# Performance work log

Measured on AMD Instinct MI355X. Metric: run time of the kernel, lower is better.

Reference implementation:

```python
import jax, jax.numpy as jnp
import numpy as np


def setup_inputs() -> dict:
    key = jax.random.key(0)
    k1, k2 = jax.random.split(key)
    B, N, M = 8, 4096, 4096
    xyz1 = jax.random.normal(k1, (B, N, 3), dtype=jnp.float32)
    xyz2 = jax.random.normal(k2, (B, M, 3), dtype=jnp.float32)
    return {"xyz1": xyz1, "xyz2": xyz2}


def _chamfer_sq_dists(xyz1, xyz2):
    # Squared euclidean all-pairs distances via ||a||^2 + ||b||^2 - 2 a.b
    # xyz1: [B,N,3], xyz2: [B,M,3]
    n1 = jnp.sum(xyz1 * xyz1, axis=-1)              # [B,N]
    n2 = jnp.sum(xyz2 * xyz2, axis=-1)              # [B,M]
    dots = jnp.einsum('bnd,bmd->bnm', xyz1, xyz2)   # [B,N,M]
    d2 = n1[:, :, None] + n2[:, None, :] - 2.0 * dots
    dist1 = jnp.min(d2, axis=2)                     # [B,N] min over xyz2
    dist2 = jnp.min(d2, axis=1)                     # [B,M] min over xyz1
    return dist1, dist2


def reference(xyz1, xyz2):
    dist1, dist2 = _chamfer_sq_dists(xyz1, xyz2)
    return jnp.mean(dist1) + jnp.mean(dist2)
```

## Files before the change

kernel.cpp:

```cpp
#include <hip/hip_runtime.h>

#define BLOCK 256
#define IPT 4
#define PTS_PER_BLOCK (BLOCK * IPT)
#define MCHUNKS 16
#define TILE_MAX 512

__global__ __launch_bounds__(BLOCK) void pack_and_init(
    const float* __restrict__ xyz1, const float* __restrict__ xyz2,
    float4* __restrict__ pk, unsigned int* __restrict__ mins,
    int n1, int ntot) {
    int i = blockIdx.x * BLOCK + threadIdx.x;
    if (i < ntot) {
        const float* s = (i < n1) ? (xyz1 + 3 * (size_t)i) : (xyz2 + 3 * (size_t)(i - n1));
        float x = s[0], y = s[1], z = s[2];
        pk[i] = make_float4(x, y, z, fmaf(z, z, fmaf(y, y, x * x)));
        mins[i] = 0x7F7F7F7Fu;
    }
}

__global__ __launch_bounds__(BLOCK) void chamfer_min_pass(
    const float4* __restrict__ pk, unsigned int* __restrict__ mins,
    int n1, int N, int M) {
    int dir = blockIdx.z;
    const float4* own = dir ? pk + n1 : pk;
    const float4* oth = dir ? pk : pk + n1;
    unsigned int* mo = dir ? mins + n1 : mins;
    int np = dir ? M : N;
    int mp = dir ? N : M;

    int bpb = np / PTS_PER_BLOCK;
    int b = blockIdx.x / bpb;
    size_t gbase = (size_t)b * np + (blockIdx.x % bpb) * PTS_PER_BLOCK + threadIdx.x;

    float4 p0 = own[gbase + 0 * BLOCK];
    float4 p1 = own[gbase + 1 * BLOCK];
    float4 p2 = own[gbase + 2 * BLOCK];
    float4 p3 = own[gbase + 3 * BLOCK];

    int mlen = mp / MCHUNKS;
    const float4* o = oth + (size_t)b * mp + (size_t)blockIdx.y * mlen;

    __shared__ float4 tile[TILE_MAX];
    for (int t = threadIdx.x; t < mlen; t += BLOCK) tile[t] = o[t];
    __syncthreads();

    float a0 = 3.0e38f, a1 = 3.0e38f, a2 = 3.0e38f, a3 = 3.0e38f;
#pragma unroll 4
    for (int j = 0; j < mlen; ++j) {
        float4 q = tile[j];
        float d0 = fmaf(p0.z, q.z, fmaf(p0.y, q.y, p0.x * q.x));
        float d1 = fmaf(p1.z, q.z, fmaf(p1.y, q.y, p1.x * q.x));
        float d2 = fmaf(p2.z, q.z, fmaf(p2.y, q.y, p2.x * q.x));
        float d3 = fmaf(p3.z, q.z, fmaf(p3.y, q.y, p3.x * q.x));
        a0 = fminf(a0, fmaf(-2.0f, d0, q.w));
        a1 = fminf(a1, fmaf(-2.0f, d1, q.w));
        a2 = fminf(a2, fmaf(-2.0f, d2, q.w));
        a3 = fminf(a3, fmaf(-2.0f, d3, q.w));
    }
    atomicMin(mo + gbase + 0 * BLOCK, __float_as_uint(fmaxf(a0 + p0.w, 0.0f)));
    atomicMin(mo + gbase + 1 * BLOCK, __float_as_uint(fmaxf(a1 + p1.w, 0.0f)));
    atomicMin(mo + gbase + 2 * BLOCK, __float_as_uint(fmaxf(a2 + p2.w, 0.0f)));
    atomicMin(mo + gbase + 3 * BLOCK, __float_as_uint(fmaxf(a3 + p3.w, 0.0f)));
}

__global__ __launch_bounds__(BLOCK) void reduce_means(
    const unsigned int* __restrict__ mins, int n1, int ntot,
    float inv1, float inv2, float* __restrict__ out) {
    float s = 0.0f;
    for (int i = blockIdx.x * BLOCK + threadIdx.x; i < ntot; i += gridDim.x * BLOCK) {
        float v = __uint_as_float(mins[i]);
        s += v * (i < n1 ? inv1 : inv2);
    }
    for (int off = 32; off; off >>= 1) s += __shfl_down(s, off, 64);
    __shared__ float red[BLOCK / 64];
    int lane = threadIdx.x & 63, wid = threadIdx.x >> 6;
    if (!lane) red[wid] = s;
    __syncthreads();
    if (!threadIdx.x) atomicAdd(out, red[0] + red[1] + red[2] + red[3]);
}

__global__ __launch_bounds__(BLOCK) void chamfer_direct(
    const float* __restrict__ x1, const float* __restrict__ x2,
    int Npts, int Mpts, float inv1, float inv2, float* __restrict__ out) {
    int dir = blockIdx.z;
    const float* own = dir ? x2 : x1;
    const float* oth = dir ? x1 : x2;
    int np = dir ? Mpts : Npts;
    int mp = dir ? Npts : Mpts;
    float scale = dir ? inv2 : inv1;

    int bpb = np / BLOCK;
    int b = blockIdx.x / bpb;
    int i = (blockIdx.x % bpb) * BLOCK + threadIdx.x;

    const float* pp = own + ((size_t)b * np + i) * 3;
    float px = pp[0], py = pp[1], pz = pp[2];
    const float* o = oth + (size_t)b * mp * 3;

    float best = 3.0e38f;
#pragma unroll 4
    for (int j = 0; j < mp; ++j) {
        float dx = px - o[3 * j + 0];
        float dy = py - o[3 * j + 1];
        float dz = pz - o[3 * j + 2];
        float d2 = fmaf(dz, dz, fmaf(dy, dy, dx * dx));
        best = fminf(best, d2);
    }
    float s = best * scale;
    for (int off = 32; off; off >>= 1) s += __shfl_down(s, off, 64);
    __shared__ float red[BLOCK / 64];
    int lane = threadIdx.x & 63, wid = threadIdx.x >> 6;
    if (!lane) red[wid] = s;
    __syncthreads();
    if (!threadIdx.x) atomicAdd(out, red[0] + red[1] + red[2] + red[3]);
}

extern "C" void kernel_launch(void* const* d_in, const int* in_sizes, int n_in,
                              void* d_out, int out_size, void* d_ws, size_t ws_size,
                              hipStream_t stream) {
    const float* xyz1 = (const float*)d_in[0];
    const float* xyz2 = (const float*)d_in[1];
    float* out = (float*)d_out;

    const int N = 4096, M = 4096;
    const int B = in_sizes[0] / (3 * N);
    const int n1 = B * N;
    const int n2 = B * M;
    const int ntot = n1 + n2;

    hipMemsetAsync(d_out, 0, sizeof(float), stream);

    size_t minBytes = (size_t)ntot * sizeof(unsigned int);
    size_t pkBytes = (size_t)ntot * sizeof(float4);
    bool okShape = (N % PTS_PER_BLOCK == 0) && (M % PTS_PER_BLOCK == 0) &&
                   (M / MCHUNKS <= TILE_MAX) && (N / MCHUNKS <= TILE_MAX);

    if (ws_size >= minBytes + pkBytes && okShape) {
        unsigned int* mins = (unsigned int*)d_ws;
        float4* pk = (float4*)((char*)d_ws + minBytes);

        pack_and_init<<<(ntot + BLOCK - 1) / BLOCK, BLOCK, 0, stream>>>(
            xyz1, xyz2, pk, mins, n1, ntot);

        dim3 grid(B * (N / PTS_PER_BLOCK), MCHUNKS, 2);
        chamfer_min_pass<<<grid, BLOCK, 0, stream>>>(pk, mins, n1, N, M);

        reduce_means<<<64, BLOCK, 0, stream>>>(mins, n1, ntot,
                                               1.0f / (float)n1, 1.0f / (float)n2, out);
    } else {
        dim3 grid(B * (N / BLOCK), 1, 2);
        chamfer_direct<<<grid, BLOCK, 0, stream>>>(xyz1, xyz2, N, M,
                                                   1.0f / (float)n1, 1.0f / (float)n2, out);
    }
}
```

Before: 39.60 us.

## Pack inner loop with f32x2 ops over SoA shared tile, fold memset into pack kernel

Stores the shared-memory tile in structure-of-arrays form and reads four candidates per float4 load, then runs the distance and min arithmetic on 2-wide float vectors so the compiler can emit packed FP32 FMA and min instructions. It also adds a launch-bounds occupancy hint and zeroes the output inside the pack kernel instead of with a separate memset. The aim is fewer VALU instructions per pair and fewer LDS loads, plus one less launch. The tile size is now fixed at compile time, so the fast path only accepts shapes where M/16 equals 256.

```diff
diff --git a/kernel.cpp b/kernel.cpp
--- a/kernel.cpp
+++ b/kernel.cpp
@@ -1,16 +1,19 @@
 #include <hip/hip_runtime.h>
+
+typedef float f32x2 __attribute__((ext_vector_type(2)));
 
 #define BLOCK 256
 #define IPT 4
 #define PTS_PER_BLOCK (BLOCK * IPT)
 #define MCHUNKS 16
-#define TILE_MAX 512
+#define TILE 256
 
 __global__ __launch_bounds__(BLOCK) void pack_and_init(
     const float* __restrict__ xyz1, const float* __restrict__ xyz2,
     float4* __restrict__ pk, unsigned int* __restrict__ mins,
-    int n1, int ntot) {
+    int n1, int ntot, float* __restrict__ out) {
     int i = blockIdx.x * BLOCK + threadIdx.x;
+    if (i == 0) *out = 0.0f;
     if (i < ntot) {
         const float* s = (i < n1) ? (xyz1 + 3 * (size_t)i) : (xyz2 + 3 * (size_t)(i - n1));
         float x = s[0], y = s[1], z = s[2];
@@ -19,7 +22,7 @@
     }
 }
 
-__global__ __launch_bounds__(BLOCK) void chamfer_min_pass(
+__global__ __launch_bounds__(BLOCK, 4) void chamfer_min_pass(
     const float4* __restrict__ pk, unsigned int* __restrict__ mins,
     int n1, int N, int M) {
     int dir = blockIdx.z;
@@ -38,30 +41,62 @@
     float4 p2 = own[gbase + 2 * BLOCK];
     float4 p3 = own[gbase + 3 * BLOCK];
 
-    int mlen = mp / MCHUNKS;
-    const float4* o = oth + (size_t)b * mp + (size_t)blockIdx.y * mlen;
+    const float4* o = oth + (size_t)b * mp + (size_t)blockIdx.y * TILE;
 
-    __shared__ float4 tile[TILE_MAX];
-    for (int t = threadIdx.x; t < mlen; t += BLOCK) tile[t] = o[t];
+    __shared__ float smem[4][TILE];
+    for (int t = threadIdx.x; t < TILE; t += BLOCK) {
+        float4 q = o[t];
+        smem[0][t] = q.x; smem[1][t] = q.y; smem[2][t] = q.z; smem[3][t] = q.w;
+    }
     __syncthreads();
 
-    float a0 = 3.0e38f, a1 = 3.0e38f, a2 = 3.0e38f, a3 = 3.0e38f;
-#pragma unroll 4
-    for (int j = 0; j < mlen; ++j) {
-        float4 q = tile[j];
-        float d0 = fmaf(p0.z, q.z, fmaf(p0.y, q.y, p0.x * q.x));
-        float d1 = fmaf(p1.z, q.z, fmaf(p1.y, q.y, p1.x * q.x));
-        float d2 = fmaf(p2.z, q.z, fmaf(p2.y, q.y, p2.x * q.x));
-        float d3 = fmaf(p3.z, q.z, fmaf(p3.y, q.y, p3.x * q.x));
-        a0 = fminf(a0, fmaf(-2.0f, d0, q.w));
-        a1 = fminf(a1, fmaf(-2.0f, d1, q.w));
-        a2 = fminf(a2, fmaf(-2.0f, d2, q.w));
-        a3 = fminf(a3, fmaf(-2.0f, d3, q.w));
+    f32x2 px0 = {p0.x, p0.x}, py0 = {p0.y, p0.y}, pz0 = {p0.z, p0.z};
+    f32x2 px1 = {p1.x, p1.x}, py1 = {p1.y, p1.y}, pz1 = {p1.z, p1.z};
+    f32x2 px2 = {p2.x, p2.x}, py2 = {p2.y, p2.y}, pz2 = {p2.z, p2.z};
+    f32x2 px3 = {p3.x, p3.x}, py3 = {p3.y, p3.y}, pz3 = {p3.z, p3.z};
+    const f32x2 m2 = {-2.0f, -2.0f};
+
+    f32x2 a0 = {3.0e38f, 3.0e38f}, a1 = a0, a2 = a0, a3 = a0;
+
+    const float4* tx4 = (const float4*)smem[0];
+    const float4* ty4 = (const float4*)smem[1];
+    const float4* tz4 = (const float4*)smem[2];
+    const float4* tw4 = (const float4*)smem[3];
+
+#pragma unroll 2
+    for (int j = 0; j < TILE / 4; ++j) {
+        float4 qx = tx4[j], qy = ty4[j], qz = tz4[j], qw = tw4[j];
+        f32x2 qxl = {qx.x, qx.y}, qxh = {qx.z, qx.w};
+        f32x2 qyl = {qy.x, qy.y}, qyh = {qy.z, qy.w};
+        f32x2 qzl = {qz.x, qz.y}, qzh = {qz.z, qz.w};
+        f32x2 qwl = {qw.x, qw.y}, qwh = {qw.z, qw.w};
+
+        f32x2 d;
+        d = qxl * px0; d = __builtin_elementwise_fma(qyl, py0, d); d = __builtin_elementwise_fma(qzl, pz0, d);
+        a0 = __builtin_elementwise_min(a0, __builtin_elementwise_fma(d, m2, qwl));
+        d = qxh * px0; d = __builtin_elementwise_fma(qyh, py0, d); d = __builtin_elementwise_fma(qzh, pz0, d);
+        a0 = __builtin_elementwise_min(a0, __builtin_elementwise_fma(d, m2, qwh));
+
+        d = qxl * px1; d = __builtin_elementwise_fma(qyl, py1, d); d = __builtin_elementwise_fma(qzl, pz1, d);
+        a1 = __builtin_elementwise_min(a1, __builtin_elementwise_fma(d, m2, qwl));
+        d = qxh * px1; d = __builtin_elementwise_fma(qyh, py1, d); d = __builtin_elementwise_fma(qzh, pz1, d);
+        a1 = __builtin_elementwise_min(a1, __builtin_elementwise_fma(d, m2, qwh));
+
+        d = qxl * px2; d = __builtin_elementwise_fma(qyl, py2, d); d = __builtin_elementwise_fma(qzl, pz2, d);
+        a2 = __builtin_elementwise_min(a2, __builtin_elementwise_fma(d, m2, qwl));
+        d = qxh * px2; d = __builtin_elementwise_fma(qyh, py2, d); d = __builtin_elementwise_fma(qzh, pz2, d);
+        a2 = __builtin_elementwise_min(a2, __builtin_elementwise_fma(d, m2, qwh));
+
+        d = qxl * px3; d = __builtin_elementwise_fma(qyl, py3, d); d = __builtin_elementwise_fma(qzl, pz3, d);
+        a3 = __builtin_elementwise_min(a3, __builtin_elementwise_fma(d, m2, qwl));
+        d = qxh * px3; d = __builtin_elementwise_fma(qyh, py3, d); d = __builtin_elementwise_fma(qzh, pz3, d);
+        a3 = __builtin_elementwise_min(a3, __builtin_elementwise_fma(d, m2, qwh));
     }
-    atomicMin(mo + gbase + 0 * BLOCK, __float_as_uint(fmaxf(a0 + p0.w, 0.0f)));
-    atomicMin(mo + gbase + 1 * BLOCK, __float_as_uint(fmaxf(a1 + p1.w, 0.0f)));
-    atomicMin(mo + gbase + 2 * BLOCK, __float_as_uint(fmaxf(a2 + p2.w, 0.0f)));
-    atomicMin(mo + gbase + 3 * BLOCK, __float_as_uint(fmaxf(a3 + p3.w, 0.0f)));
+
+    atomicMin(mo + gbase + 0 * BLOCK, __float_as_uint(fmaxf(fminf(a0.x, a0.y) + p0.w, 0.0f)));
+    atomicMin(mo + gbase + 1 * BLOCK, __float_as_uint(fmaxf(fminf(a1.x, a1.y) + p1.w, 0.0f)));
+    atomicMin(mo + gbase + 2 * BLOCK, __float_as_uint(fmaxf(fminf(a2.x, a2.y) + p2.w, 0.0f)));
+    atomicMin(mo + gbase + 3 * BLOCK, __float_as_uint(fmaxf(fminf(a3.x, a3.y) + p3.w, 0.0f)));
 }
 
 __global__ __launch_bounds__(BLOCK) void reduce_means(
@@ -129,19 +164,17 @@
     const int n2 = B * M;
     const int ntot = n1 + n2;
 
-    hipMemsetAsync(d_out, 0, sizeof(float), stream);
-
     size_t minBytes = (size_t)ntot * sizeof(unsigned int);
     size_t pkBytes = (size_t)ntot * sizeof(float4);
     bool okShape = (N % PTS_PER_BLOCK == 0) && (M % PTS_PER_BLOCK == 0) &&
-                   (M / MCHUNKS <= TILE_MAX) && (N / MCHUNKS <= TILE_MAX);
+                   (M / MCHUNKS == TILE) && (N / MCHUNKS == TILE);
 
     if (ws_size >= minBytes + pkBytes && okShape) {
         unsigned int* mins = (unsigned int*)d_ws;
         float4* pk = (float4*)((char*)d_ws + minBytes);
 
         pack_and_init<<<(ntot + BLOCK - 1) / BLOCK, BLOCK, 0, stream>>>(
-            xyz1, xyz2, pk, mins, n1, ntot);
+            xyz1, xyz2, pk, mins, n1, ntot, out);
 
         dim3 grid(B * (N / PTS_PER_BLOCK), MCHUNKS, 2);
         chamfer_min_pass<<<grid, BLOCK, 0, stream>>>(pk, mins, n1, N, M);
@@ -149,6 +182,7 @@
         reduce_means<<<64, BLOCK, 0, stream>>>(mins, n1, ntot,
                                                1.0f / (float)n1, 1.0f / (float)n2, out);
     } else {
+        hipMemsetAsync(d_out, 0, sizeof(float), stream);
         dim3 grid(B * (N / BLOCK), 1, 2);
         chamfer_direct<<<grid, BLOCK, 0, stream>>>(xyz1, xyz2, N, M,
                                                    1.0f / (float)n1, 1.0f / (float)n2, out);
```

After: 37.65 us. 1.05x faster.

## Compute chamfer distances with bf16 split-precision MFMA and fused reduction

Applied to the files above, without the earlier changes.

Replaces the scalar FMA all-pairs loop with 32x32x16 bf16 MFMA instructions. Each coordinate is split into high and low bf16 parts so the dot product plus the other point's norm is recovered at near-fp32 accuracy. Row minima are reduced in registers and across lanes, then summed straight into the output, which removes the atomicMin buffer, the separate reduce kernel and the memset. In exchange it adds packing overhead and risks small accuracy loss, and it uses a fixed grid of 256 blocks with each block streaming the whole other cloud.

```diff
diff --git a/kernel.cpp b/kernel.cpp
--- a/kernel.cpp
+++ b/kernel.cpp
@@ -1,83 +1,140 @@
 #include <hip/hip_runtime.h>
 
+typedef float f32x16 __attribute__((ext_vector_type(16)));
+typedef short bf16x8 __attribute__((ext_vector_type(8)));
+
 #define BLOCK 256
-#define IPT 4
-#define PTS_PER_BLOCK (BLOCK * IPT)
-#define MCHUNKS 16
-#define TILE_MAX 512
-
-__global__ __launch_bounds__(BLOCK) void pack_and_init(
-    const float* __restrict__ xyz1, const float* __restrict__ xyz2,
-    float4* __restrict__ pk, unsigned int* __restrict__ mins,
-    int n1, int ntot) {
+#define NPTS 4096
+#define CHUNK_PTS 256
+#define NCHUNK (NPTS / CHUNK_PTS)
+#define SUBS (CHUNK_PTS / 32)
+#define TW 2
+#define TILES_PER_BLOCK 8
+
+__device__ inline unsigned int f2bf(float x) {
+    unsigned int u = __float_as_uint(x);
+    return (u + 0x7FFFu + ((u >> 16) & 1)) >> 16;
+}
+__device__ inline float bf2f(unsigned int b) { return __uint_as_float(b << 16); }
+__device__ inline unsigned int pk2(unsigned int lo, unsigned int hi) {
+    return (hi << 16) | (lo & 0xFFFFu);
+}
+
+__global__ __launch_bounds__(BLOCK) void pack_pts(
+    const float* __restrict__ x1, const float* __restrict__ x2,
+    uint4* __restrict__ arrA, uint4* __restrict__ arrB,
+    float* __restrict__ wn, int n1, int ntot, float* __restrict__ out) {
     int i = blockIdx.x * BLOCK + threadIdx.x;
-    if (i < ntot) {
-        const float* s = (i < n1) ? (xyz1 + 3 * (size_t)i) : (xyz2 + 3 * (size_t)(i - n1));
-        float x = s[0], y = s[1], z = s[2];
-        pk[i] = make_float4(x, y, z, fmaf(z, z, fmaf(y, y, x * x)));
-        mins[i] = 0x7F7F7F7Fu;
-    }
-}
-
-__global__ __launch_bounds__(BLOCK) void chamfer_min_pass(
-    const float4* __restrict__ pk, unsigned int* __restrict__ mins,
-    int n1, int N, int M) {
-    int dir = blockIdx.z;
-    const float4* own = dir ? pk + n1 : pk;
-    const float4* oth = dir ? pk : pk + n1;
-    unsigned int* mo = dir ? mins + n1 : mins;
-    int np = dir ? M : N;
-    int mp = dir ? N : M;
-
-    int bpb = np / PTS_PER_BLOCK;
-    int b = blockIdx.x / bpb;
-    size_t gbase = (size_t)b * np + (blockIdx.x % bpb) * PTS_PER_BLOCK + threadIdx.x;
-
-    float4 p0 = own[gbase + 0 * BLOCK];
-    float4 p1 = own[gbase + 1 * BLOCK];
-    float4 p2 = own[gbase + 2 * BLOCK];
-    float4 p3 = own[gbase + 3 * BLOCK];
-
-    int mlen = mp / MCHUNKS;
-    const float4* o = oth + (size_t)b * mp + (size_t)blockIdx.y * mlen;
-
-    __shared__ float4 tile[TILE_MAX];
-    for (int t = threadIdx.x; t < mlen; t += BLOCK) tile[t] = o[t];
+    if (i == 0) out[0] = 0.0f;
+    if (i >= ntot) return;
+    const float* s = (i < n1) ? x1 + 3 * (size_t)i : x2 + 3 * (size_t)(i - n1);
+    float x = s[0], y = s[1], z = s[2];
+    float w = fmaf(z, z, fmaf(y, y, x * x));
+    wn[i] = w;
+    unsigned int hx = f2bf(x), hy = f2bf(y), hz = f2bf(z);
+    unsigned int lx = f2bf(x - bf2f(hx)), ly = f2bf(y - bf2f(hy)), lz = f2bf(z - bf2f(hz));
+    unsigned int hw = f2bf(w), lw = f2bf(w - bf2f(hw));
+    unsigned int ax = f2bf(-2.f * bf2f(hx)), ay = f2bf(-2.f * bf2f(hy)), az = f2bf(-2.f * bf2f(hz));
+    unsigned int bx = f2bf(-2.f * bf2f(lx)), by = f2bf(-2.f * bf2f(ly)), bz = f2bf(-2.f * bf2f(lz));
+    const unsigned int one = 0x3F80u;
+    uint4 A0 = make_uint4(pk2(ax, ay), pk2(az, bx), pk2(by, bz), pk2(ax, ay));
+    uint4 A1 = make_uint4(pk2(az, one), pk2(one, 0u), 0u, 0u);
+    arrA[(size_t)i * 2 + 0] = A0;
+    arrA[(size_t)i * 2 + 1] = A1;
+    uint4 B0 = make_uint4(pk2(hx, hy), pk2(hz, hx), pk2(hy, hz), pk2(lx, ly));
+    uint4 B1 = make_uint4(pk2(lz, hw), pk2(lw, 0u), 0u, 0u);
+    arrB[(size_t)i * 2 + 0] = B0;
+    arrB[(size_t)i * 2 + 1] = B1;
+}
+
+__global__ __launch_bounds__(BLOCK) void chamfer_mfma(
+    const uint4* __restrict__ arrA, const uint4* __restrict__ arrB,
+    const float* __restrict__ wn, int n1, int Bc,
+    float inv1, float inv2, float* __restrict__ out) {
+    __shared__ uint4 lds[CHUNK_PTS * 2];
+    __shared__ float red[4];
+    int tid = threadIdx.x;
+    int lane = tid & 63, widx = tid >> 6;
+    int l31 = lane & 31, blk = lane >> 5;
+
+    int bid = blockIdx.x;
+    int bd = bid >> 4;
+    int seg = bid & 15;
+    int dir = (bd >= Bc) ? 1 : 0;
+    int b = dir ? bd - Bc : bd;
+    int ownOff = dir ? n1 : 0;
+    int othOff = dir ? 0 : n1;
+    float inv = dir ? inv2 : inv1;
+
+    int tile0 = seg * TILES_PER_BLOCK + widx * TW;
+    int row0 = tile0 * 32;
+
+    size_t aBase = (size_t)(ownOff + b * NPTS + row0 + l31) * 2 + blk;
+    bf16x8 afA = *(const bf16x8*)(arrA + aBase);
+    bf16x8 afB = *(const bf16x8*)(arrA + aBase + 64);
+
+    const uint4* gB = arrB + (size_t)(othOff + b * NPTS) * 2;
+
+    f32x16 runA, runB;
+#pragma unroll
+    for (int r = 0; r < 16; ++r) { runA[r] = 3.0e38f; runB[r] = 3.0e38f; }
+
+    uint4 p0 = gB[tid], p1 = gB[tid + 256];
+    lds[tid] = p0;
+    lds[tid + 256] = p1;
     __syncthreads();
 
-    float a0 = 3.0e38f, a1 = 3.0e38f, a2 = 3.0e38f, a3 = 3.0e38f;
-#pragma unroll 4
-    for (int j = 0; j < mlen; ++j) {
-        float4 q = tile[j];
-        float d0 = fmaf(p0.z, q.z, fmaf(p0.y, q.y, p0.x * q.x));
-        float d1 = fmaf(p1.z, q.z, fmaf(p1.y, q.y, p1.x * q.x));
-        float d2 = fmaf(p2.z, q.z, fmaf(p2.y, q.y, p2.x * q.x));
-        float d3 = fmaf(p3.z, q.z, fmaf(p3.y, q.y, p3.x * q.x));
-        a0 = fminf(a0, fmaf(-2.0f, d0, q.w));
-        a1 = fminf(a1, fmaf(-2.0f, d1, q.w));
-        a2 = fminf(a2, fmaf(-2.0f, d2, q.w));
-        a3 = fminf(a3, fmaf(-2.0f, d3, q.w));
-    }
-    atomicMin(mo + gbase + 0 * BLOCK, __float_as_uint(fmaxf(a0 + p0.w, 0.0f)));
-    atomicMin(mo + gbase + 1 * BLOCK, __float_as_uint(fmaxf(a1 + p1.w, 0.0f)));
-    atomicMin(mo + gbase + 2 * BLOCK, __float_as_uint(fmaxf(a2 + p2.w, 0.0f)));
-    atomicMin(mo + gbase + 3 * BLOCK, __float_as_uint(fmaxf(a3 + p3.w, 0.0f)));
-}
-
-__global__ __launch_bounds__(BLOCK) void reduce_means(
-    const unsigned int* __restrict__ mins, int n1, int ntot,
-    float inv1, float inv2, float* __restrict__ out) {
-    float s = 0.0f;
-    for (int i = blockIdx.x * BLOCK + threadIdx.x; i < ntot; i += gridDim.x * BLOCK) {
-        float v = __uint_as_float(mins[i]);
-        s += v * (i < n1 ? inv1 : inv2);
-    }
-    for (int off = 32; off; off >>= 1) s += __shfl_down(s, off, 64);
-    __shared__ float red[BLOCK / 64];
-    int lane = threadIdx.x & 63, wid = threadIdx.x >> 6;
-    if (!lane) red[wid] = s;
+    f32x16 zero = {};
+    for (int c = 0; c < NCHUNK; ++c) {
+        if (c + 1 < NCHUNK) {
+            p0 = gB[(c + 1) * 512 + tid];
+            p1 = gB[(c + 1) * 512 + 256 + tid];
+        }
+        const bf16x8* lp = (const bf16x8*)lds;
+#pragma unroll
+        for (int s = 0; s < SUBS; s += 2) {
+            bf16x8 bf0 = lp[(s * 32 + l31) * 2 + blk];
+            bf16x8 bf1 = lp[((s + 1) * 32 + l31) * 2 + blk];
+            f32x16 acc0a = __builtin_amdgcn_mfma_f32_32x32x16_bf16(afA, bf0, zero, 0, 0, 0);
+            f32x16 acc0b = __builtin_amdgcn_mfma_f32_32x32x16_bf16(afB, bf0, zero, 0, 0, 0);
+            f32x16 acc1a = __builtin_amdgcn_mfma_f32_32x32x16_bf16(afA, bf1, zero, 0, 0, 0);
+            f32x16 acc1b = __builtin_amdgcn_mfma_f32_32x32x16_bf16(afB, bf1, zero, 0, 0, 0);
+#pragma unroll
+            for (int r = 0; r < 16; ++r) {
+                runA[r] = fminf(runA[r], fminf(acc0a[r], acc1a[r]));
+                runB[r] = fminf(runB[r], fminf(acc0b[r], acc1b[r]));
+            }
+        }
+        __syncthreads();
+        if (c + 1 < NCHUNK) {
+            lds[tid] = p0;
+            lds[tid + 256] = p1;
+        }
+        __syncthreads();
+    }
+
+#pragma unroll
+    for (int m = 1; m <= 16; m <<= 1) {
+#pragma unroll
+        for (int r = 0; r < 16; ++r) {
+            runA[r] = fminf(runA[r], __shfl_xor(runA[r], m, 64));
+            runB[r] = fminf(runB[r], __shfl_xor(runB[r], m, 64));
+        }
+    }
+    float contrib = 0.0f;
+    if (l31 == 0) {
+        const float* wp = wn + ownOff + b * NPTS;
+#pragma unroll
+        for (int r = 0; r < 16; ++r) {
+            int rowA = row0 + ((r & 3) + 8 * (r >> 2) + 4 * blk);
+            contrib += runA[r] + wp[rowA];
+            contrib += runB[r] + wp[rowA + 32];
+        }
+    }
+    contrib += __shfl_xor(contrib, 32, 64);
+    if (lane == 0) red[widx] = contrib * inv;
     __syncthreads();
-    if (!threadIdx.x) atomicAdd(out, red[0] + red[1] + red[2] + red[3]);
+    if (tid == 0) atomicAdd(out, red[0] + red[1] + red[2] + red[3]);
 }
 
 __global__ __launch_bounds__(BLOCK) void chamfer_direct(
@@ -123,34 +180,29 @@
     const float* xyz2 = (const float*)d_in[1];
     float* out = (float*)d_out;
 
-    const int N = 4096, M = 4096;
-    const int B = in_sizes[0] / (3 * N);
-    const int n1 = B * N;
-    const int n2 = B * M;
+    const int Bc = in_sizes[0] / (3 * NPTS);
+    const int n1 = Bc * NPTS;
+    const int n2 = Bc * NPTS;
     const int ntot = n1 + n2;
 
-    hipMemsetAsync(d_out, 0, sizeof(float), stream);
-
-    size_t minBytes = (size_t)ntot * sizeof(unsigned int);
-    size_t pkBytes = (size_t)ntot * sizeof(float4);
-    bool okShape = (N % PTS_PER_BLOCK == 0) && (M % PTS_PER_BLOCK == 0) &&
-                   (M / MCHUNKS <= TILE_MAX) && (N / MCHUNKS <= TILE_MAX);
-
-    if (ws_size >= minBytes + pkBytes && okShape) {
-        unsigned int* mins = (unsigned int*)d_ws;
-        float4* pk = (float4*)((char*)d_ws + minBytes);
-
-        pack_and_init<<<(ntot + BLOCK - 1) / BLOCK, BLOCK, 0, stream>>>(
-            xyz1, xyz2, pk, mins, n1, ntot);
-
-        dim3 grid(B * (N / PTS_PER_BLOCK), MCHUNKS, 2);
-        chamfer_min_pass<<<grid, BLOCK, 0, stream>>>(pk, mins, n1, N, M);
-
-        reduce_means<<<64, BLOCK, 0, stream>>>(mins, n1, ntot,
-                                               1.0f / (float)n1, 1.0f / (float)n2, out);
+    size_t need = (size_t)ntot * (32 + 32 + 4);
+    bool okShape = Bc >= 1 && in_sizes[0] == Bc * 3 * NPTS && in_sizes[1] == in_sizes[0];
+
+    if (okShape && ws_size >= need) {
+        uint4* arrA = (uint4*)d_ws;
+        uint4* arrB = (uint4*)((char*)d_ws + (size_t)ntot * 32);
+        float* wn = (float*)((char*)d_ws + (size_t)ntot * 64);
+
+        pack_pts<<<(ntot + BLOCK - 1) / BLOCK, BLOCK, 0, stream>>>(
+            xyz1, xyz2, arrA, arrB, wn, n1, ntot, out);
+
+        chamfer_mfma<<<Bc * 2 * 16, BLOCK, 0, stream>>>(
+            arrA, arrB, wn, n1, Bc,
+            1.0f / (float)n1, 1.0f / (float)n2, out);
     } else {
-        dim3 grid(B * (N / BLOCK), 1, 2);
-        chamfer_direct<<<grid, BLOCK, 0, stream>>>(xyz1, xyz2, N, M,
+        hipMemsetAsync(d_out, 0, sizeof(float), stream);
+        dim3 grid((in_sizes[0] / 3 / NPTS) * (NPTS / BLOCK), 1, 2);
+        chamfer_direct<<<grid, BLOCK, 0, stream>>>(xyz1, xyz2, NPTS, NPTS,
                                                    1.0f / (float)n1, 1.0f / (float)n2, out);
     }
 }
```

Measured after the change: 46.51 us. +17.5%, slower.
